# Performance work log

Hardware: AMD Instinct MI355X
Metric: run time of the kernel (lower is better)

## Reference

```python
import jax, jax.numpy as jnp
import numpy as np

B, C, H, W = 4, 512, 64, 64
R = 8
D = C // R  # inner channels = 64


def setup_inputs() -> dict:
    key = jax.random.key(0)
    k1, k2, k3 = jax.random.split(key, 3)
    x = jax.random.normal(k1, (B, C, H, W), dtype=jnp.float32)
    # 1x1 conv weights, stored as [out, in] (kernel spatial dims are 1)
    w_qkv = jax.random.normal(k2, (3 * D, C), dtype=jnp.float32) * (1.0 / np.sqrt(C))
    w_out = jax.random.normal(k3, (C, D), dtype=jnp.float32) * (1.0 / np.sqrt(D))
    # nn.Parameter(torch.zeros(1)) in the original; use nonzero so output != input
    scale = jnp.array([0.3], dtype=jnp.float32)
    return {"x": x, "w_qkv": w_qkv, "w_out": w_out, "scale": scale}


def reference(x, w_qkv, w_out, scale):
    b, c, h, w = x.shape
    hw = h * w
    # 1x1 conv == channel matmul
    t = jnp.einsum('oc,bchw->bohw', w_qkv, x)  # [B, 3D, H, W]
    d = t.shape[1] // 3
    key_ = t[:, :d].reshape(b, d, hw)      # chunk order: key, query, value
    query = t[:, d:2 * d].reshape(b, d, hw)
    value = t[:, 2 * d:].reshape(b, d, hw)
    # scores[b, k, q] = sum_d key[b,d,k] * query[b,d,q]
    scores = jnp.einsum('bdk,bdq->bkq', key_, query)  # [B, hw, hw]
    # NB: original uses Softmax(dim=1) -> normalize over the KEY axis
    attn = jax.nn.softmax(scores, axis=1)
    out = jnp.einsum('bdk,bkq->bdq', value, attn)     # [B, D, hw]
    out = out.reshape(b, d, h, w)
    out = jnp.einsum('oc,bchw->bohw', w_out, out)     # [B, C, H, W]
    return scale * out + x
```

## Files before the change

### kernel.cpp

```cpp
#include <hip/hip_runtime.h>

#define B_ 4
#define C_ 512
#define D_ 64
#define HW_ 4096
#define NCHUNK 4
#define KT_PER_CHUNK 16

typedef __attribute__((ext_vector_type(8))) short bf16x8;
typedef __attribute__((ext_vector_type(4))) float f32x4;

__device__ __forceinline__ unsigned short f2bf(float f) {
    unsigned int u = __builtin_bit_cast(unsigned int, f);
    u += 0x7fffu + ((u >> 16) & 1u);
    return (unsigned short)(u >> 16);
}

#if __has_builtin(__builtin_amdgcn_exp2f)
#define EXP2(x) __builtin_amdgcn_exp2f(x)
#else
#define EXP2(x) __expf((x) * 0.6931471805599453f)
#endif

#define OFF_WQKV 0u
#define OFF_WOUT 196608u
#define OFF_PART 262144u
#define OFF_KT   17039360u
#define OFF_QT   19136512u
#define OFF_V    21233664u
#define OFF_ML   25427968u

__global__ __launch_bounds__(256) void k_convw(const float* __restrict__ wqkv,
                                               const float* __restrict__ wout,
                                               unsigned short* __restrict__ wq_b,
                                               unsigned short* __restrict__ wo_b) {
    int i = blockIdx.x * 256 + threadIdx.x;
    if (i < 192 * C_) wq_b[i] = f2bf(wqkv[i]);
    if (i < C_ * D_)  wo_b[i] = f2bf(wout[i]);
}

__global__ __launch_bounds__(256) void k_qkv(const float* __restrict__ x,
                                             const unsigned short* __restrict__ wq,
                                             unsigned short* __restrict__ kt,
                                             unsigned short* __restrict__ qt,
                                             unsigned short* __restrict__ v) {
    __shared__ float tile[64][65];
    __shared__ unsigned short xb[64][64];
    int pT = blockIdx.x, b = blockIdx.y;
    int tid = threadIdx.x, wid = tid >> 6, lane = tid & 63;
    int g = lane >> 4, r16 = lane & 15;
    int pc = tid & 63, grp = tid >> 6;
    int pl = tid >> 2, ch = tid & 3;

    f32x4 acc[3][4] = {};
    for (int ct = 0; ct < 8; ++ct) {
        int c0 = ct * 64;
        __syncthreads();
        #pragma unroll
        for (int r = 0; r < 16; ++r) {
            int cl = grp * 16 + r;
            tile[cl][pc] = x[(size_t)(b * C_ + c0 + cl) * HW_ + pT * 64 + pc];
        }
        __syncthreads();
        unsigned int packed[8];
        #pragma unroll
        for (int j = 0; j < 8; ++j) {
            unsigned short lo = f2bf(tile[ch * 16 + 2 * j][pl]);
            unsigned short hi = f2bf(tile[ch * 16 + 2 * j + 1][pl]);
            packed[j] = (unsigned)lo | ((unsigned)hi << 16);
        }
        {
            unsigned short* rowp = &xb[pl][0];
            int swz = pl & 7;
            *(uint4*)(rowp + (((ch * 2)     ^ swz) << 3)) =
                make_uint4(packed[0], packed[1], packed[2], packed[3]);
            *(uint4*)(rowp + (((ch * 2 + 1) ^ swz) << 3)) =
                make_uint4(packed[4], packed[5], packed[6], packed[7]);
        }
        __syncthreads();
        #pragma unroll
        for (int cs = 0; cs < 2; ++cs) {
            bf16x8 bb[4];
            #pragma unroll
            for (int ps = 0; ps < 4; ++ps) {
                int row = ps * 16 + r16;
                bb[ps] = *(const bf16x8*)(&xb[row][0] + (((cs * 4 + g) ^ (row & 7)) << 3));
            }
            #pragma unroll
            for (int ot = 0; ot < 3; ++ot) {
                bf16x8 a = *(const bf16x8*)(wq + (size_t)(wid * 48 + ot * 16 + r16) * C_
                                            + c0 + cs * 32 + g * 8);
                #pragma unroll
                for (int ps = 0; ps < 4; ++ps)
                    acc[ot][ps] = __builtin_amdgcn_mfma_f32_16x16x32_bf16(a, bb[ps], acc[ot][ps], 0, 0, 0);
            }
        }
    }
    #pragma unroll
    for (int ot = 0; ot < 3; ++ot) {
        int obase = wid * 48 + ot * 16;
        int oT = obase >> 6;
        int dbase = (obase & 63) + 4 * g;
        #pragma unroll
        for (int ps = 0; ps < 4; ++ps) {
            int pp = pT * 64 + ps * 16 + r16;
            if (oT < 2) {
                unsigned short* dst = (oT == 0) ? kt : qt;
                float qs = (oT == 1) ? 1.4426950408889634f : 1.0f;
                unsigned int u0 = f2bf(acc[ot][ps][0] * qs) | ((unsigned)f2bf(acc[ot][ps][1] * qs) << 16);
                unsigned int u1 = f2bf(acc[ot][ps][2] * qs) | ((unsigned)f2bf(acc[ot][ps][3] * qs) << 16);
                *reinterpret_cast<uint2*>(dst + (size_t)(b * HW_ + pp) * D_ + dbase) =
                    make_uint2(u0, u1);
            } else {
                #pragma unroll
                for (int r = 0; r < 4; ++r)
                    v[(size_t)(b * D_ + dbase + r) * HW_ + pp] = f2bf(acc[ot][ps][r]);
            }
        }
    }
}

__global__ __launch_bounds__(256, 4) void k_attn(const unsigned short* __restrict__ kt,
                                                 const unsigned short* __restrict__ qt,
                                                 const unsigned short* __restrict__ v,
                                                 float* __restrict__ part,
                                                 float* __restrict__ ml) {
    __shared__ unsigned short klds[2][64][64];
    __shared__ unsigned short vlds[2][64][64];
    __shared__ unsigned short plds[4][16][64];
    int qT = blockIdx.x, chunk = blockIdx.y, b = blockIdx.z;
    int tid = threadIdx.x, wid = tid >> 6, lane = tid & 63;
    int g = lane >> 4, r16 = lane & 15;
    int q0 = qT * 64 + wid * 16;

    const unsigned short* qp = qt + (size_t)(b * HW_ + q0 + r16) * D_ + g * 8;
    bf16x8 qf0 = *(const bf16x8*)(qp);
    bf16x8 qf1 = *(const bf16x8*)(qp + 32);

    int isV = tid >> 7, tt = tid & 127;
    int srow = tt >> 1, shalf = tt & 1;
    const unsigned short* sbase = isV
        ? (v  + (size_t)b * D_ * HW_ + (size_t)srow * HW_ + shalf * 32)
        : (kt + (size_t)b * HW_ * D_ + (size_t)srow * D_  + shalf * 32);
    const int smul = isV ? 1 : D_;
    const int k0 = chunk * (KT_PER_CHUNK * 64);

    uint4 rr0, rr1, rr2, rr3;
    auto gload = [&](int t) {
        const uint4* s = (const uint4*)(sbase + (size_t)(k0 + t * 64) * smul);
        rr0 = s[0]; rr1 = s[1]; rr2 = s[2]; rr3 = s[3];
    };
    auto swrite = [&](int buf) {
        unsigned short* Lb = isV ? &vlds[buf][0][0] : &klds[buf][0][0];
        unsigned short* rowp = Lb + srow * 64;
        int swz = srow & 7, c0 = shalf * 4;
        *(uint4*)(rowp + (((c0 + 0) ^ swz) << 3)) = rr0;
        *(uint4*)(rowp + (((c0 + 1) ^ swz) << 3)) = rr1;
        *(uint4*)(rowp + (((c0 + 2) ^ swz) << 3)) = rr2;
        *(uint4*)(rowp + (((c0 + 3) ^ swz) << 3)) = rr3;
    };

    gload(0);
    swrite(0);
    gload(1);
    __syncthreads();

    f32x4 acc[4] = {};
    float m = -3.0e38f, lsum = 0.f;
    int cur = 0;
    unsigned short* pb = &plds[wid][0][0];

    for (int t = 0; t < KT_PER_CHUNK; ++t) {
        if (t + 1 < KT_PER_CHUNK) swrite(cur ^ 1);
        if (t + 2 < KT_PER_CHUNK) gload(t + 2);

        f32x4 s4v[4];
        #pragma unroll
        for (int ks = 0; ks < 4; ++ks) {
            int row = ks * 16 + r16;
            const unsigned short* rp = &klds[cur][0][0] + row * 64;
            int swz = row & 7;
            bf16x8 kf0 = *(const bf16x8*)(rp + ((g ^ swz) << 3));
            bf16x8 kf1 = *(const bf16x8*)(rp + (((g + 4) ^ swz) << 3));
            f32x4 z = {};
            z = __builtin_amdgcn_mfma_f32_16x16x32_bf16(kf0, qf0, z, 0, 0, 0);
            z = __builtin_amdgcn_mfma_f32_16x16x32_bf16(kf1, qf1, z, 0, 0, 0);
            s4v[ks] = z;
        }
        float tmax = s4v[0][0];
        #pragma unroll
        for (int ks = 0; ks < 4; ++ks)
            #pragma unroll
            for (int r = 0; r < 4; ++r) tmax = fmaxf(tmax, s4v[ks][r]);
        tmax = fmaxf(tmax, __shfl_xor(tmax, 16));
        tmax = fmaxf(tmax, __shfl_xor(tmax, 32));
        float mnew = fmaxf(m, tmax);
        float al = EXP2(m - mnew);
        float tsum = 0.f;
        #pragma unroll
        for (int ks = 0; ks < 4; ++ks) {
            float e0 = EXP2(s4v[ks][0] - mnew);
            float e1 = EXP2(s4v[ks][1] - mnew);
            float e2 = EXP2(s4v[ks][2] - mnew);
            float e3 = EXP2(s4v[ks][3] - mnew);
            tsum += (e0 + e1) + (e2 + e3);
            unsigned int u0 = f2bf(e0) | ((unsigned)f2bf(e1) << 16);
            unsigned int u1 = f2bf(e2) | ((unsigned)f2bf(e3) << 16);
            int ch = (2 * ks + (g >> 1)) ^ (r16 & 7);
            *(uint2*)(pb + r16 * 64 + (ch << 3) + 4 * (g & 1)) = make_uint2(u0, u1);
        }
        tsum += __shfl_xor(tsum, 16);
        tsum += __shfl_xor(tsum, 32);
        lsum = lsum * al + tsum;
        #pragma unroll
        for (int dt = 0; dt < 4; ++dt) {
            acc[dt][0] *= al; acc[dt][1] *= al; acc[dt][2] *= al; acc[dt][3] *= al;
        }
        m = mnew;
        asm volatile("s_waitcnt lgkmcnt(0)" ::: "memory");
        int pswz = r16 & 7;
        bf16x8 pf0 = *(const bf16x8*)(pb + r16 * 64 + ((g ^ pswz) << 3));
        bf16x8 pf1 = *(const bf16x8*)(pb + r16 * 64 + (((g + 4) ^ pswz) << 3));
        #pragma unroll
        for (int dt = 0; dt < 4; ++dt) {
            int row = dt * 16 + r16;
            const unsigned short* rp = &vlds[cur][0][0] + row * 64;
            int swz = row & 7;
            bf16x8 vf0 = *(const bf16x8*)(rp + ((g ^ swz) << 3));
            bf16x8 vf1 = *(const bf16x8*)(rp + (((g + 4) ^ swz) << 3));
            acc[dt] = __builtin_amdgcn_mfma_f32_16x16x32_bf16(vf0, pf0, acc[dt], 0, 0, 0);
            acc[dt] = __builtin_amdgcn_mfma_f32_16x16x32_bf16(vf1, pf1, acc[dt], 0, 0, 0);
        }
        __syncthreads();
        cur ^= 1;
    }

    int row = ((b * NCHUNK + chunk) * HW_) + q0 + r16;
    #pragma unroll
    for (int dt = 0; dt < 4; ++dt)
        *reinterpret_cast<f32x4*>(&part[(size_t)row * D_ + dt * 16 + 4 * g]) = acc[dt];
    if (g == 0) {
        ml[2 * row]     = m;
        ml[2 * row + 1] = lsum;
    }
}

__global__ __launch_bounds__(256) void k_out(const unsigned short* __restrict__ wo,
                                             const float* __restrict__ part,
                                             const float* __restrict__ ml,
                                             const float* __restrict__ x,
                                             const float* __restrict__ scale,
                                             float* __restrict__ out) {
    __shared__ unsigned short alds[64][64];
    int pT = blockIdx.x, b = blockIdx.y;
    int tid = threadIdx.x;
    {
        int pl = tid >> 2, dg = tid & 3;
        int q = pT * 64 + pl;
        float wi[NCHUNK];
        {
            float mi[NCHUNK], li[NCHUNK];
            #pragma unroll
            for (int i = 0; i < NCHUNK; ++i) {
                int row = (b * NCHUNK + i) * HW_ + q;
                mi[i] = ml[2 * row];
                li[i] = ml[2 * row + 1];
            }
            float M = mi[0];
            #pragma unroll
            for (int i = 1; i < NCHUNK; ++i) M = fmaxf(M, mi[i]);
            float L = 0.f;
            #pragma unroll
            for (int i = 0; i < NCHUNK; ++i) {
                wi[i] = EXP2(mi[i] - M);
                L += wi[i] * li[i];
            }
            float invL = 1.0f / L;
            #pragma unroll
            for (int i = 0; i < NCHUNK; ++i) wi[i] *= invL;
        }
        unsigned int packed[8];
        #pragma unroll
        for (int j = 0; j < 4; ++j) {
            f32x4 o = {};
            #pragma unroll
            for (int i = 0; i < NCHUNK; ++i) {
                const f32x4 pv = *(const f32x4*)&part[
                    (size_t)((b * NCHUNK + i) * HW_ + q) * D_ + dg * 16 + 4 * j];
                o[0] += wi[i] * pv[0]; o[1] += wi[i] * pv[1];
                o[2] += wi[i] * pv[2]; o[3] += wi[i] * pv[3];
            }
            packed[2 * j]     = f2bf(o[0]) | ((unsigned)f2bf(o[1]) << 16);
            packed[2 * j + 1] = f2bf(o[2]) | ((unsigned)f2bf(o[3]) << 16);
        }
        unsigned short* rowp = &alds[pl][0];
        int swz = pl & 7;
        *(uint4*)(rowp + (((dg * 2)     ^ swz) << 3)) =
            make_uint4(packed[0], packed[1], packed[2], packed[3]);
        *(uint4*)(rowp + (((dg * 2 + 1) ^ swz) << 3)) =
            make_uint4(packed[4], packed[5], packed[6], packed[7]);
    }
    __syncthreads();
    int wid = tid >> 6, lane = tid & 63;
    int g = lane >> 4, r16 = lane & 15;
    float sc = scale[0];
    bf16x8 bfr[4][2];
    #pragma unroll
    for (int ps = 0; ps < 4; ++ps) {
        int row = ps * 16 + r16;
        const unsigned short* rp = &alds[row][0];
        int swz = row & 7;
        bfr[ps][0] = *(const bf16x8*)(rp + (((0 * 4 + g) ^ swz) << 3));
        bfr[ps][1] = *(const bf16x8*)(rp + (((1 * 4 + g) ^ swz) << 3));
    }
    #pragma unroll 2
    for (int ot = 0; ot < 8; ++ot) {
        int orow = wid * 128 + ot * 16;
        bf16x8 a0 = *(const bf16x8*)(wo + (size_t)(orow + r16) * D_ + g * 8);
        bf16x8 a1 = *(const bf16x8*)(wo + (size_t)(orow + r16) * D_ + 32 + g * 8);
        #pragma unroll
        for (int ps = 0; ps < 4; ++ps) {
            f32x4 acc = {};
            acc = __builtin_amdgcn_mfma_f32_16x16x32_bf16(a0, bfr[ps][0], acc, 0, 0, 0);
            acc = __builtin_amdgcn_mfma_f32_16x16x32_bf16(a1, bfr[ps][1], acc, 0, 0, 0);
            int o = orow + 4 * g;
            int pp = pT * 64 + ps * 16 + r16;
            size_t base = (size_t)(b * C_ + o) * HW_ + pp;
            #pragma unroll
            for (int r = 0; r < 4; ++r)
                out[base + (size_t)r * HW_] = sc * acc[r] + x[base + (size_t)r * HW_];
        }
    }
}

extern "C" void kernel_launch(void* const* d_in, const int* in_sizes, int n_in,
                              void* d_out, int out_size, void* d_ws, size_t ws_size,
                              hipStream_t stream) {
    const float* x     = (const float*)d_in[0];
    const float* wqkv  = (const float*)d_in[1];
    const float* wout  = (const float*)d_in[2];
    const float* scale = (const float*)d_in[3];
    char* ws = (char*)d_ws;
    unsigned short* wq_b = (unsigned short*)(ws + OFF_WQKV);
    unsigned short* wo_b = (unsigned short*)(ws + OFF_WOUT);
    float*          prt  = (float*)(ws + OFF_PART);
    unsigned short* ktb  = (unsigned short*)(ws + OFF_KT);
    unsigned short* qtb  = (unsigned short*)(ws + OFF_QT);
    unsigned short* vb   = (unsigned short*)(ws + OFF_V);
    float*          mlb  = (float*)(ws + OFF_ML);

    hipLaunchKernelGGL(k_convw, dim3(384), dim3(256), 0, stream, wqkv, wout, wq_b, wo_b);
    hipLaunchKernelGGL(k_qkv,   dim3(64, 4),    dim3(256), 0, stream, x, wq_b, ktb, qtb, vb);
    hipLaunchKernelGGL(k_attn,  dim3(64, NCHUNK, 4), dim3(256), 0, stream, ktb, qtb, vb, prt, mlb);
    hipLaunchKernelGGL(k_out,   dim3(64, 4),    dim3(256), 0, stream, wo_b, prt, mlb, x, scale,
                       (float*)d_out);
}
```

Measured before the change: 95.12 us.

## Halve pixel tile in qkv/out kernels and prefetch x into registers

The qkv projection and output projection kernels now process 32 pixels per block instead of 64, doubling the grid from 256 to 512 blocks so more CUs are occupied on the memory-bound phases. The qkv kernel also loads the next channel tile of x into registers while the current tile is being converted and multiplied, and drops one barrier per iteration. In exchange, each block reuses each weight load across fewer pixels, so weight traffic per pixel rises and x rows are read in shorter 128-byte segments.

```diff
diff --git a/kernel.cpp b/kernel.cpp
--- a/kernel.cpp
+++ b/kernel.cpp
@@ -44,54 +44,53 @@
                                              unsigned short* __restrict__ kt,
                                              unsigned short* __restrict__ qt,
                                              unsigned short* __restrict__ v) {
-    __shared__ float tile[64][65];
-    __shared__ unsigned short xb[64][64];
+    __shared__ float tile[64][33];
+    __shared__ unsigned short xb[32][64];
     int pT = blockIdx.x, b = blockIdx.y;
     int tid = threadIdx.x, wid = tid >> 6, lane = tid & 63;
     int g = lane >> 4, r16 = lane & 15;
-    int pc = tid & 63, grp = tid >> 6;
-    int pl = tid >> 2, ch = tid & 3;
-
-    f32x4 acc[3][4] = {};
+    int pp0 = pT * 32;
+    int lp = tid & 31, lc = tid >> 5;
+    int pl = tid >> 3, ch = tid & 7;
+
+    float rx[8];
+    auto gload = [&](int ct) {
+        #pragma unroll
+        for (int r = 0; r < 8; ++r)
+            rx[r] = x[(size_t)(b * C_ + ct * 64 + lc * 8 + r) * HW_ + pp0 + lp];
+    };
+
+    f32x4 acc[3][2] = {};
+    gload(0);
     for (int ct = 0; ct < 8; ++ct) {
-        int c0 = ct * 64;
+        #pragma unroll
+        for (int r = 0; r < 8; ++r) tile[lc * 8 + r][lp] = rx[r];
         __syncthreads();
-        #pragma unroll
-        for (int r = 0; r < 16; ++r) {
-            int cl = grp * 16 + r;
-            tile[cl][pc] = x[(size_t)(b * C_ + c0 + cl) * HW_ + pT * 64 + pc];
-        }
+        unsigned int pk[4];
+        #pragma unroll
+        for (int j = 0; j < 4; ++j) {
+            unsigned short lo = f2bf(tile[ch * 8 + 2 * j][pl]);
+            unsigned short hi = f2bf(tile[ch * 8 + 2 * j + 1][pl]);
+            pk[j] = (unsigned)lo | ((unsigned)hi << 16);
+        }
+        *(uint4*)(&xb[pl][0] + ((ch ^ (pl & 7)) << 3)) =
+            make_uint4(pk[0], pk[1], pk[2], pk[3]);
+        if (ct + 1 < 8) gload(ct + 1);
         __syncthreads();
-        unsigned int packed[8];
-        #pragma unroll
-        for (int j = 0; j < 8; ++j) {
-            unsigned short lo = f2bf(tile[ch * 16 + 2 * j][pl]);
-            unsigned short hi = f2bf(tile[ch * 16 + 2 * j + 1][pl]);
-            packed[j] = (unsigned)lo | ((unsigned)hi << 16);
-        }
-        {
-            unsigned short* rowp = &xb[pl][0];
-            int swz = pl & 7;
-            *(uint4*)(rowp + (((ch * 2)     ^ swz) << 3)) =
-                make_uint4(packed[0], packed[1], packed[2], packed[3]);
-            *(uint4*)(rowp + (((ch * 2 + 1) ^ swz) << 3)) =
-                make_uint4(packed[4], packed[5], packed[6], packed[7]);
-        }
-        __syncthreads();
         #pragma unroll
         for (int cs = 0; cs < 2; ++cs) {
-            bf16x8 bb[4];
-            #pragma unroll
-            for (int ps = 0; ps < 4; ++ps) {
+            bf16x8 bb[2];
+            #pragma unroll
+            for (int ps = 0; ps < 2; ++ps) {
                 int row = ps * 16 + r16;
                 bb[ps] = *(const bf16x8*)(&xb[row][0] + (((cs * 4 + g) ^ (row & 7)) << 3));
             }
             #pragma unroll
             for (int ot = 0; ot < 3; ++ot) {
                 bf16x8 a = *(const bf16x8*)(wq + (size_t)(wid * 48 + ot * 16 + r16) * C_
-                                            + c0 + cs * 32 + g * 8);
+                                            + ct * 64 + cs * 32 + g * 8);
                 #pragma unroll
-                for (int ps = 0; ps < 4; ++ps)
+                for (int ps = 0; ps < 2; ++ps)
                     acc[ot][ps] = __builtin_amdgcn_mfma_f32_16x16x32_bf16(a, bb[ps], acc[ot][ps], 0, 0, 0);
             }
         }
@@ -102,8 +101,8 @@
         int oT = obase >> 6;
         int dbase = (obase & 63) + 4 * g;
         #pragma unroll
-        for (int ps = 0; ps < 4; ++ps) {
-            int pp = pT * 64 + ps * 16 + r16;
+        for (int ps = 0; ps < 2; ++ps) {
+            int pp = pp0 + ps * 16 + r16;
             if (oT < 2) {
                 unsigned short* dst = (oT == 0) ? kt : qt;
                 float qs = (oT == 1) ? 1.4426950408889634f : 1.0f;
@@ -251,12 +250,13 @@
                                              const float* __restrict__ x,
                                              const float* __restrict__ scale,
                                              float* __restrict__ out) {
-    __shared__ unsigned short alds[64][64];
+    __shared__ unsigned short alds[32][64];
     int pT = blockIdx.x, b = blockIdx.y;
     int tid = threadIdx.x;
+    int pp0 = pT * 32;
     {
-        int pl = tid >> 2, dg = tid & 3;
-        int q = pT * 64 + pl;
+        int pl = tid >> 3, dgg = tid & 7;
+        int q = pp0 + pl;
         float wi[NCHUNK];
         {
             float mi[NCHUNK], li[NCHUNK];
@@ -279,34 +279,31 @@
             #pragma unroll
             for (int i = 0; i < NCHUNK; ++i) wi[i] *= invL;
         }
-        unsigned int packed[8];
-        #pragma unroll
-        for (int j = 0; j < 4; ++j) {
-            f32x4 o = {};
-            #pragma unroll
-            for (int i = 0; i < NCHUNK; ++i) {
-                const f32x4 pv = *(const f32x4*)&part[
-                    (size_t)((b * NCHUNK + i) * HW_ + q) * D_ + dg * 16 + 4 * j];
-                o[0] += wi[i] * pv[0]; o[1] += wi[i] * pv[1];
-                o[2] += wi[i] * pv[2]; o[3] += wi[i] * pv[3];
-            }
-            packed[2 * j]     = f2bf(o[0]) | ((unsigned)f2bf(o[1]) << 16);
-            packed[2 * j + 1] = f2bf(o[2]) | ((unsigned)f2bf(o[3]) << 16);
-        }
-        unsigned short* rowp = &alds[pl][0];
-        int swz = pl & 7;
-        *(uint4*)(rowp + (((dg * 2)     ^ swz) << 3)) =
-            make_uint4(packed[0], packed[1], packed[2], packed[3]);
-        *(uint4*)(rowp + (((dg * 2 + 1) ^ swz) << 3)) =
-            make_uint4(packed[4], packed[5], packed[6], packed[7]);
+        float o8[8] = {};
+        #pragma unroll
+        for (int i = 0; i < NCHUNK; ++i) {
+            const float* pvp = &part[(size_t)((b * NCHUNK + i) * HW_ + q) * D_ + dgg * 8];
+            f32x4 pv0 = *(const f32x4*)(pvp);
+            f32x4 pv1 = *(const f32x4*)(pvp + 4);
+            o8[0] += wi[i] * pv0[0]; o8[1] += wi[i] * pv0[1];
+            o8[2] += wi[i] * pv0[2]; o8[3] += wi[i] * pv0[3];
+            o8[4] += wi[i] * pv1[0]; o8[5] += wi[i] * pv1[1];
+            o8[6] += wi[i] * pv1[2]; o8[7] += wi[i] * pv1[3];
+        }
+        unsigned int pk[4];
+        #pragma unroll
+        for (int j = 0; j < 4; ++j)
+            pk[j] = (unsigned)f2bf(o8[2 * j]) | ((unsigned)f2bf(o8[2 * j + 1]) << 16);
+        *(uint4*)(&alds[pl][0] + ((dgg ^ (pl & 7)) << 3)) =
+            make_uint4(pk[0], pk[1], pk[2], pk[3]);
     }
     __syncthreads();
     int wid = tid >> 6, lane = tid & 63;
     int g = lane >> 4, r16 = lane & 15;
     float sc = scale[0];
-    bf16x8 bfr[4][2];
+    bf16x8 bfr[2][2];
     #pragma unroll
-    for (int ps = 0; ps < 4; ++ps) {
+    for (int ps = 0; ps < 2; ++ps) {
         int row = ps * 16 + r16;
         const unsigned short* rp = &alds[row][0];
         int swz = row & 7;
@@ -319,12 +316,12 @@
         bf16x8 a0 = *(const bf16x8*)(wo + (size_t)(orow + r16) * D_ + g * 8);
         bf16x8 a1 = *(const bf16x8*)(wo + (size_t)(orow + r16) * D_ + 32 + g * 8);
         #pragma unroll
-        for (int ps = 0; ps < 4; ++ps) {
+        for (int ps = 0; ps < 2; ++ps) {
             f32x4 acc = {};
             acc = __builtin_amdgcn_mfma_f32_16x16x32_bf16(a0, bfr[ps][0], acc, 0, 0, 0);
             acc = __builtin_amdgcn_mfma_f32_16x16x32_bf16(a1, bfr[ps][1], acc, 0, 0, 0);
             int o = orow + 4 * g;
-            int pp = pT * 64 + ps * 16 + r16;
+            int pp = pp0 + ps * 16 + r16;
             size_t base = (size_t)(b * C_ + o) * HW_ + pp;
             #pragma unroll
             for (int r = 0; r < 4; ++r)
@@ -350,8 +347,8 @@
     float*          mlb  = (float*)(ws + OFF_ML);
 
     hipLaunchKernelGGL(k_convw, dim3(384), dim3(256), 0, stream, wqkv, wout, wq_b, wo_b);
-    hipLaunchKernelGGL(k_qkv,   dim3(64, 4),    dim3(256), 0, stream, x, wq_b, ktb, qtb, vb);
+    hipLaunchKernelGGL(k_qkv,   dim3(128, 4),   dim3(256), 0, stream, x, wq_b, ktb, qtb, vb);
     hipLaunchKernelGGL(k_attn,  dim3(64, NCHUNK, 4), dim3(256), 0, stream, ktb, qtb, vb, prt, mlb);
-    hipLaunchKernelGGL(k_out,   dim3(64, 4),    dim3(256), 0, stream, wo_b, prt, mlb, x, scale,
+    hipLaunchKernelGGL(k_out,   dim3(128, 4),   dim3(256), 0, stream, wo_b, prt, mlb, x, scale,
                        (float*)d_out);
 }
```

Measured after the change: 84.05 us. -11.6%, faster.
